# Performance work log

Measured on AMD Instinct MI355X. Metric: run time of the kernel, lower is better.

## Reference

```python
import jax, jax.numpy as jnp
import numpy as np

N, M = 1024, 32
FN, FE = 64, 32
AGG_N, AGG_E = 128, 64
OUT_N, OUT_E = 64, 32


def _build_indices(n, m):
    nip, eip = [], []
    k = 0
    for i in range(1, n):
        j0 = max(0, i - m)
        nip += list(range(j0, i))
        eip += list(range(k, k + i - j0))
        k += i - j0
    n1 = np.array(nip, np.int32)
    eT = np.array(eip, np.int32)
    n2 = np.concatenate([np.full(min(i, m), i, np.int32) for i in range(1, n)])
    # padded previous-node window indices (0 = zero pad slot)
    prev_nodes = np.zeros(n * m, np.int32)
    k = 0
    for i in range(n):
        t = min(i, m)
        prev_nodes[(i + 1) * m - t:(i + 1) * m] = np.arange(k, k + t) + 1
        k += t
    n_e = k
    norm_node = np.full(n, 1.0 / m, np.float32)
    for i in range(1, m):
        norm_node[i] = 1.0 / i
    prev_edges = np.zeros(n_e * m, np.int32)
    k = 0
    e = 0
    for i in range(n):
        j0 = max(0, i - m)
        for j in range(j0, i):
            if j > j0:
                prev_edges[(e + 1) * m - (j - j0):(e + 1) * m] = np.arange(k, k + j - j0) + 1
            e += 1
        k += i - j0
    norm_edge = np.ones(n_e, np.float32)
    k = 0
    for i in range(1, n):
        t = min(i, m)
        for j in range(t):
            if j > 0:
                norm_edge[k] = 1.0 / j
            k += 1
    return n1, eT, n2, prev_nodes, norm_node, prev_edges, norm_edge, n_e

N1, ET, N2, PREV_N, NORM_N, PREV_E, NORM_E, NE = _build_indices(N, M)
N1 = jnp.asarray(N1); ET = jnp.asarray(ET); N2 = jnp.asarray(N2)
PREV_N = jnp.asarray(PREV_N); PREV_E = jnp.asarray(PREV_E)
NORM_N = jnp.asarray(NORM_N); NORM_E = jnp.asarray(NORM_E)


def setup_inputs() -> dict:
    key = jax.random.key(0)
    ks = jax.random.split(key, 20)
    s = 0.02
    inp = {
        'input_nodes': jax.random.normal(ks[0], (2, N, FN), jnp.float32),
        'input_edges': jax.random.normal(ks[1], (2, NE, FE), jnp.float32),
        # node-branch MLPs (exclude_last=False)
        'Wan1': jax.random.normal(ks[2], (2 * FN + FE, 2 * AGG_N)) * s,
        'ban1': jnp.zeros((2 * AGG_N,)),
        'Wan2': jax.random.normal(ks[3], (2 * AGG_N, AGG_N)) * s,
        'ban2': jnp.zeros((AGG_N,)),
        'Wln1': jax.random.normal(ks[4], (AGG_N + FN, AGG_N + FN)) * s,
        'bln1': jnp.zeros((AGG_N + FN,)),
        'Wln2': jax.random.normal(ks[5], (AGG_N + FN, OUT_N)) * s,
        'bln2': jnp.zeros((OUT_N,)),
        # edge-branch MLPs
        'Wae1': jax.random.normal(ks[6], (FN + FE, 2 * AGG_E)) * s,
        'bae1': jnp.zeros((2 * AGG_E,)),
        'Wae2': jax.random.normal(ks[7], (2 * AGG_E, AGG_E)) * s,
        'bae2': jnp.zeros((AGG_E,)),
        'Wle1': jax.random.normal(ks[8], (AGG_E + FE, AGG_E + FE)) * s,
        'ble1': jnp.zeros((AGG_E + FE,)),
        'Wle2': jax.random.normal(ks[9], (AGG_E + FE, OUT_E)) * s,
        'ble2': jnp.zeros((OUT_E,)),
    }
    return inp


def _mlp2(x, W1, b1, W2, b2):
    return jax.nn.relu(jax.nn.relu(x @ W1 + b1) @ W2 + b2)


def reference(input_nodes, input_edges, Wan1, ban1, Wan2, ban2, Wln1, bln1, Wln2, bln2,
              Wae1, bae1, Wae2, bae2, Wle1, ble1, Wle2, ble2):
    B = input_nodes.shape[0]
    # gather node-edge pairs [B, NE, FN+FE] and node-edge-node triples [B, NE, 2FN+FE]
    pairs = jnp.concatenate([input_nodes[:, N1], input_edges[:, ET]], axis=-1)
    triples = jnp.concatenate([input_nodes[:, N1], input_edges[:, ET], input_nodes[:, N2]], axis=-1)
    # node branch (exclude_last=False -> triples)
    hn = _mlp2(triples, Wan1, ban1, Wan2, ban2)                     # [B, NE, AGG_N]
    hn = jnp.concatenate([jnp.zeros((B, 1, AGG_N), hn.dtype), hn], axis=1)
    pn = hn[:, PREV_N].reshape(B, N, M, AGG_N).sum(axis=2)          # padded window sum
    pn = pn * NORM_N[None, :, None]
    nodes_in = jnp.concatenate([pn, input_nodes], axis=-1)
    out_nodes = _mlp2(nodes_in, Wln1, bln1, Wln2, bln2)             # activation_nodes = relu
    # edge branch (pairs)
    he = _mlp2(pairs, Wae1, bae1, Wae2, bae2)                       # [B, NE, AGG_E]
    he = jnp.concatenate([jnp.zeros((B, 1, AGG_E), he.dtype), he], axis=1)
    pe = he[:, PREV_E].reshape(B, NE, M, AGG_E).sum(axis=2)
    pe = pe * NORM_E[None, :, None]
    edges_in = jnp.concatenate([pe, input_edges], axis=-1)
    out_edges = _mlp2(edges_in, Wle1, ble1, Wle2, ble2)             # activation_edges = relu
    return out_nodes, out_edges
```

## Files before the change

### kernel.cpp

```cpp
#include <hip/hip_runtime.h>
#include <cstdint>

#define NN    1024
#define MM    32
#define NEDGE 32240
#define MROWS 64480
#define PX    168
#define PST   392

typedef unsigned short ushort_t;

typedef __bf16 bf16x8 __attribute__((ext_vector_type(8)));
typedef float  floatx4 __attribute__((ext_vector_type(4)));

__device__ __forceinline__ float b2f(ushort_t u) {
    union { unsigned int i; float f; } v; v.i = ((unsigned int)u) << 16; return v.f;
}
__device__ __forceinline__ ushort_t f2b(float f) {
    unsigned int u = __builtin_bit_cast(unsigned int, f);
    u = (u + 0x7FFFu + ((u >> 16) & 1u)) >> 16;
    return (ushort_t)u;
}
__device__ __forceinline__ int edge_base(int i) {
    return (i <= MM) ? ((i * (i - 1)) >> 1) : (496 + (i - MM) * MM);
}
__device__ __forceinline__ void edge_ij(int e, int& i, int& j) {
    if (e < 496) {
        i = (int)((1.0f + sqrtf(8.0f * (float)e + 1.0f)) * 0.5f);
        while (((i * (i - 1)) >> 1) > e) --i;
        while (((i * (i + 1)) >> 1) <= e) ++i;
        j = e - ((i * (i - 1)) >> 1);
    } else {
        int q = e - 496;
        i = MM + (q >> 5);
        j = i - MM + (q & 31);
    }
}

__global__ __launch_bounds__(256) void k_pack(
        const float* an1, const float* an2, const float* ae1, const float* ae2,
        const float* le1, const float* le2, const float* ln1, const float* ln2,
        const float* nodes, const float* edges,
        ushort_t* pan1, ushort_t* pan2, ushort_t* pae1, ushort_t* pae2,
        ushort_t* ple1, ushort_t* ple2, ushort_t* pln1, ushort_t* pln2,
        ushort_t* nodesb, ushort_t* edgesb, int2* ijt) {
    __shared__ float tile[32][33];
    const int bid = blockIdx.x;
    const int tid = threadIdx.x;
    if (bid < 152) {
        const float* s; ushort_t* d; int K, N, t;
        if (bid < 40)       { s = an1; d = pan1; K = 160; N = 256; t = bid;       }
        else if (bid < 72)  { s = an2; d = pan2; K = 256; N = 128; t = bid - 40;  }
        else if (bid < 84)  { s = ae1; d = pae1; K = 96;  N = 128; t = bid - 72;  }
        else if (bid < 92)  { s = ae2; d = pae2; K = 128; N = 64;  t = bid - 84;  }
        else if (bid < 101) { s = le1; d = ple1; K = 96;  N = 96;  t = bid - 92;  }
        else if (bid < 104) { s = le2; d = ple2; K = 96;  N = 32;  t = bid - 101; }
        else if (bid < 140) { s = ln1; d = pln1; K = 192; N = 192; t = bid - 104; }
        else                { s = ln2; d = pln2; K = 192; N = 64;  t = bid - 140; }
        int ntn = N >> 5;
        int tk = t / ntn, tn = t - tk * ntn;
        int k0 = tk * 32, n0 = tn * 32;
        int tx = tid & 31, ty = tid >> 5;
#pragma unroll
        for (int m = 0; m < 4; ++m)
            tile[ty + m * 8][tx] = s[(size_t)(k0 + ty + m * 8) * N + n0 + tx];
        __syncthreads();
#pragma unroll
        for (int m = 0; m < 4; ++m)
            d[(size_t)(n0 + ty + m * 8) * K + k0 + tx] = f2b(tile[tx][ty + m * 8]);
    } else if (bid < 280) {
        int i4 = (bid - 152) * 256 + tid;
        float4 v = ((const float4*)nodes)[i4];
        uint2 o;
        o.x = (unsigned)f2b(v.x) | ((unsigned)f2b(v.y) << 16);
        o.y = (unsigned)f2b(v.z) | ((unsigned)f2b(v.w) << 16);
        ((uint2*)nodesb)[i4] = o;
    } else if (bid < 2296) {
        int i4 = (bid - 280) * 256 + tid;
        if (i4 < 515840) {
            float4 v = ((const float4*)edges)[i4];
            uint2 o;
            o.x = (unsigned)f2b(v.x) | ((unsigned)f2b(v.y) << 16);
            o.y = (unsigned)f2b(v.z) | ((unsigned)f2b(v.w) << 16);
            ((uint2*)edgesb)[i4] = o;
        }
    } else {
        int e = (bid - 2296) * 256 + tid;
        if (e < NEDGE) { int i, j; edge_ij(e, i, j); ijt[e] = make_int2(i, j); }
    }
}

__global__ __launch_bounds__(512, 2) void k_agg(
        const ushort_t* __restrict__ nodesb, const ushort_t* __restrict__ edgesb,
        const int2* __restrict__ ijt,
        const ushort_t* __restrict__ pan1, const float* __restrict__ ban1,
        const ushort_t* __restrict__ pan2, const float* __restrict__ ban2,
        const ushort_t* __restrict__ pae1, const float* __restrict__ bae1,
        const ushort_t* __restrict__ pae2, const float* __restrict__ bae2,
        ushort_t* __restrict__ hn, ushort_t* __restrict__ he) {
    __shared__ alignas(16) ushort_t X[32 * PX];
    __shared__ alignas(16) ushort_t H[32 * PST];
    const int tid = threadIdx.x;
    const int w = tid >> 6, l = tid & 63, lrow = l & 15, lq = l >> 4;
    const int mt = blockIdx.x;
    floatx4 zero = {0.f, 0.f, 0.f, 0.f};

    bf16x8 B0[5], B1[5], B2[3];
#pragma unroll
    for (int kt = 0; kt < 5; ++kt) {
        B0[kt] = *(const bf16x8*)(pan1 + (size_t)(16 * w + lrow) * 160 + kt * 32 + lq * 8);
        B1[kt] = *(const bf16x8*)(pan1 + (size_t)(16 * (w + 8) + lrow) * 160 + kt * 32 + lq * 8);
    }
#pragma unroll
    for (int kt = 0; kt < 3; ++kt)
        B2[kt] = *(const bf16x8*)(pae1 + (size_t)(16 * w + lrow) * 96 + kt * 32 + lq * 8);
    float c0 = ban1[16 * w + lrow];
    float c1 = ban1[16 * (w + 8) + lrow];
    float c2 = bae1[16 * w + lrow];

#pragma unroll
    for (int k = 0; k < 4; ++k) {
        int rr = w * 4 + k;
        int r = mt * 32 + rr;
        int off = (r >= NEDGE) ? 1 : 0;
        int2 ij = ijt[r - off * NEDGE];
        int bN = off * NN;
        unsigned* xr = (unsigned*)(X + rr * PX);
        const unsigned* nj = (const unsigned*)(nodesb + (size_t)(bN + ij.y) * 64);
        const unsigned* ni = (const unsigned*)(nodesb + (size_t)(bN + ij.x) * 64);
        const unsigned* eb = (const unsigned*)(edgesb + (size_t)r * 32);
        if (l < 32) { xr[l] = nj[l]; xr[48 + l] = ni[l]; }
        else        xr[l] = eb[l - 32];
    }
    __syncthreads();

#pragma unroll
    for (int s = 0; s < 2; ++s) {
        bf16x8 A[5];
#pragma unroll
        for (int kt = 0; kt < 5; ++kt)
            A[kt] = *(const bf16x8*)&X[(s * 16 + lrow) * PX + kt * 32 + lq * 8];
        floatx4 a0 = zero, a1 = zero, a2 = zero;
#pragma unroll
        for (int kt = 0; kt < 5; ++kt) {
            a0 = __builtin_amdgcn_mfma_f32_16x16x32_bf16(A[kt], B0[kt], a0, 0, 0, 0);
            a1 = __builtin_amdgcn_mfma_f32_16x16x32_bf16(A[kt], B1[kt], a1, 0, 0, 0);
        }
#pragma unroll
        for (int kt = 0; kt < 3; ++kt)
            a2 = __builtin_amdgcn_mfma_f32_16x16x32_bf16(A[kt], B2[kt], a2, 0, 0, 0);
#pragma unroll
        for (int r_ = 0; r_ < 4; ++r_) {
            int row = (s * 16 + lq * 4 + r_) * PST;
            H[row + 16 * w + lrow]       = f2b(fmaxf(a0[r_] + c0, 0.f));
            H[row + 128 + 16 * w + lrow] = f2b(fmaxf(a1[r_] + c1, 0.f));
            H[row + 256 + 16 * w + lrow] = f2b(fmaxf(a2[r_] + c2, 0.f));
        }
    }
    __syncthreads();

    floatx4 o0[2], o1[2];
    if (w < 4) {
        bf16x8 D0[8], D1[8];
#pragma unroll
        for (int kt = 0; kt < 8; ++kt) {
            D0[kt] = *(const bf16x8*)(pan2 + (size_t)(16 * w + lrow) * 256 + kt * 32 + lq * 8);
            D1[kt] = *(const bf16x8*)(pan2 + (size_t)(16 * (w + 4) + lrow) * 256 + kt * 32 + lq * 8);
        }
        float d0 = ban2[16 * w + lrow];
        float d1 = ban2[16 * (w + 4) + lrow];
#pragma unroll
        for (int s = 0; s < 2; ++s) {
            floatx4 a0 = zero, a1 = zero;
#pragma unroll
            for (int kt = 0; kt < 8; ++kt) {
                bf16x8 a = *(const bf16x8*)&H[(s * 16 + lrow) * PST + kt * 32 + lq * 8];
                a0 = __builtin_amdgcn_mfma_f32_16x16x32_bf16(a, D0[kt], a0, 0, 0, 0);
                a1 = __builtin_amdgcn_mfma_f32_16x16x32_bf16(a, D1[kt], a1, 0, 0, 0);
            }
#pragma unroll
            for (int r_ = 0; r_ < 4; ++r_) { o0[s][r_] = a0[r_] + d0; o1[s][r_] = a1[r_] + d1; }
        }
    } else {
        int u = w - 4;
        bf16x8 E[4];
#pragma unroll
        for (int kt = 0; kt < 4; ++kt)
            E[kt] = *(const bf16x8*)(pae2 + (size_t)(16 * u + lrow) * 128 + kt * 32 + lq * 8);
        float d2 = bae2[16 * u + lrow];
#pragma unroll
        for (int s = 0; s < 2; ++s) {
            floatx4 a2 = zero;
#pragma unroll
            for (int kt = 0; kt < 4; ++kt) {
                bf16x8 a = *(const bf16x8*)&H[(s * 16 + lrow) * PST + 256 + kt * 32 + lq * 8];
                a2 = __builtin_amdgcn_mfma_f32_16x16x32_bf16(a, E[kt], a2, 0, 0, 0);
            }
#pragma unroll
            for (int r_ = 0; r_ < 4; ++r_) o0[s][r_] = a2[r_] + d2;
        }
    }
    __syncthreads();

    ushort_t* S = X;
    ushort_t* T = H;
    if (w < 4) {
#pragma unroll
        for (int s = 0; s < 2; ++s)
#pragma unroll
            for (int r_ = 0; r_ < 4; ++r_) {
                int row = (s * 16 + lq * 4 + r_) * 136;
                S[row + 16 * w + lrow]        = f2b(fmaxf(o0[s][r_], 0.f));
                S[row + 64 + 16 * w + lrow]   = f2b(fmaxf(o1[s][r_], 0.f));
            }
    } else {
        int u = w - 4;
#pragma unroll
        for (int s = 0; s < 2; ++s)
#pragma unroll
            for (int r_ = 0; r_ < 4; ++r_)
                T[(s * 16 + lq * 4 + r_) * 72 + 16 * u + lrow] = f2b(fmaxf(o0[s][r_], 0.f));
    }
    __syncthreads();

    {
        int row = tid >> 4, c = tid & 15;
        ((uint4*)(hn + (size_t)(mt * 32 + row) * 128))[c] = *(const uint4*)&S[row * 136 + c * 8];
        if (tid < 256) {
            int row2 = tid >> 3, c2 = tid & 7;
            ((uint4*)(he + (size_t)(mt * 32 + row2) * 64))[c2] = *(const uint4*)&T[row2 * 72 + c2 * 8];
        }
    }
}

__global__ __launch_bounds__(256) void k_mid(
        const ushort_t* __restrict__ hn, const ushort_t* __restrict__ he,
        ushort_t* __restrict__ pn, ushort_t* __restrict__ pre) {
    const int tid = threadIdx.x;
    if (blockIdx.x < 2048) {
        int ri = blockIdx.x;
        int b = ri >> 10, i = ri & 1023;
        int t = min(i, MM);
        int base = b * NEDGE + edge_base(i);
        int c = tid & 63, g = tid >> 6;
        float s0 = 0.f, s1 = 0.f;
        for (int p = g; p < t; p += 4) {
            unsigned u = ((const unsigned*)(hn + (size_t)(base + p) * 128))[c];
            s0 += b2f((ushort_t)(u & 0xffff));
            s1 += b2f((ushort_t)(u >> 16));
        }
        __shared__ float red[4][128];
        red[g][c * 2] = s0; red[g][c * 2 + 1] = s1;
        __syncthreads();
        if (tid < 64) {
            float inv = 1.0f / (float)max(t, 1);
            float a0 = (red[0][tid * 2] + red[1][tid * 2] + red[2][tid * 2] + red[3][tid * 2]) * inv;
            float a1 = (red[0][tid * 2 + 1] + red[1][tid * 2 + 1] + red[2][tid * 2 + 1] + red[3][tid * 2 + 1]) * inv;
            ((unsigned*)(pn + (size_t)ri * 128))[tid] = (unsigned)f2b(a0) | ((unsigned)f2b(a1) << 16);
        }
    } else {
        int bi = blockIdx.x - 2048;
        int b = bi >> 10, i = bi & 1023;
        int t = min(i, MM);
        if (t == 0) return;
        int base = b * NEDGE + edge_base(i);
        __shared__ alignas(16) ushort_t hw[32 * 64];
        for (int u = tid; u < t * 8; u += 256)
            ((uint4*)hw)[u] = ((const uint4*)he)[(size_t)base * 8 + u];
        __syncthreads();
        if (tid < 64) {
            float run = 0.f;
            for (int p = 0; p < t; ++p) {
                float v = (p == 0) ? 0.f : run / (float)p;
                pre[(size_t)(base + p) * 64 + tid] = f2b(v);
                run += b2f(hw[p * 64 + tid]);
            }
        }
    }
}

__global__ __launch_bounds__(192) void k_final(
        const ushort_t* __restrict__ pn, const ushort_t* __restrict__ nodesb,
        const ushort_t* __restrict__ pln1, const float* __restrict__ bln1,
        const ushort_t* __restrict__ pln2, const float* __restrict__ bln2,
        float* __restrict__ out_nodes,
        const ushort_t* __restrict__ pre, const ushort_t* __restrict__ edgesb,
        const ushort_t* __restrict__ ple1, const float* __restrict__ ble1,
        const ushort_t* __restrict__ ple2, const float* __restrict__ ble2,
        float* __restrict__ out_edges) {
    __shared__ alignas(16) ushort_t LA[32 * 200];
    __shared__ alignas(16) ushort_t LB[32 * 200];
    const int tid = threadIdx.x;
    const int w = tid >> 6, l = tid & 63, lrow = l & 15, lq = l >> 4;
    floatx4 zero = {0.f, 0.f, 0.f, 0.f};

    if (blockIdx.x < 64) {
        int tile = blockIdx.x;
        for (int u = tid; u < 768; u += 192) {
            int row = u / 24, c = u - row * 24;
            int r = tile * 32 + row;
            const uint4* src = (c < 16) ? ((const uint4*)(pn + (size_t)r * 128) + c)
                                        : ((const uint4*)(nodesb + (size_t)r * 64) + (c - 16));
            *(uint4*)&LA[row * 200 + c * 8] = *src;
        }
        bf16x8 f1[6][4]; float v1[4];
#pragma unroll
        for (int kt = 0; kt < 6; ++kt)
#pragma unroll
            for (int nt = 0; nt < 4; ++nt)
                f1[kt][nt] = *(const bf16x8*)(pln1 + (size_t)(w * 64 + nt * 16 + lrow) * 192 + kt * 32 + lq * 8);
#pragma unroll
        for (int nt = 0; nt < 4; ++nt) v1[nt] = bln1[w * 64 + nt * 16 + lrow];
        __syncthreads();

        floatx4 acc[2][4];
#pragma unroll
        for (int s = 0; s < 2; ++s)
#pragma unroll
            for (int nt = 0; nt < 4; ++nt) acc[s][nt] = zero;
#pragma unroll
        for (int s = 0; s < 2; ++s)
#pragma unroll
            for (int kt = 0; kt < 6; ++kt) {
                bf16x8 a = *(const bf16x8*)&LA[(s * 16 + lrow) * 200 + kt * 32 + lq * 8];
#pragma unroll
                for (int nt = 0; nt < 4; ++nt)
                    acc[s][nt] = __builtin_amdgcn_mfma_f32_16x16x32_bf16(a, f1[kt][nt], acc[s][nt], 0, 0, 0);
            }
#pragma unroll
        for (int s = 0; s < 2; ++s)
#pragma unroll
            for (int nt = 0; nt < 4; ++nt) {
                int col = w * 64 + nt * 16 + lrow;
#pragma unroll
                for (int r_ = 0; r_ < 4; ++r_)
                    LB[(s * 16 + lq * 4 + r_) * 200 + col] = f2b(fmaxf(acc[s][nt][r_] + v1[nt], 0.f));
            }
        bf16x8 f2[6][2]; float v2[2] = {0.f, 0.f};
        if (w < 2) {
#pragma unroll
            for (int kt = 0; kt < 6; ++kt)
#pragma unroll
                for (int nt = 0; nt < 2; ++nt)
                    f2[kt][nt] = *(const bf16x8*)(pln2 + (size_t)(w * 32 + nt * 16 + lrow) * 192 + kt * 32 + lq * 8);
#pragma unroll
            for (int nt = 0; nt < 2; ++nt) v2[nt] = bln2[w * 32 + nt * 16 + lrow];
        }
        __syncthreads();
        if (w < 2) {
            floatx4 a2[2][2];
#pragma unroll
            for (int s = 0; s < 2; ++s) { a2[s][0] = zero; a2[s][1] = zero; }
#pragma unroll
            for (int s = 0; s < 2; ++s)
#pragma unroll
                for (int kt = 0; kt < 6; ++kt) {
                    bf16x8 a = *(const bf16x8*)&LB[(s * 16 + lrow) * 200 + kt * 32 + lq * 8];
#pragma unroll
                    for (int nt = 0; nt < 2; ++nt)
                        a2[s][nt] = __builtin_amdgcn_mfma_f32_16x16x32_bf16(a, f2[kt][nt], a2[s][nt], 0, 0, 0);
                }
#pragma unroll
            for (int s = 0; s < 2; ++s)
#pragma unroll
                for (int nt = 0; nt < 2; ++nt) {
                    int col = w * 32 + nt * 16 + lrow;
#pragma unroll
                    for (int r_ = 0; r_ < 4; ++r_)
                        out_nodes[(size_t)(tile * 32 + s * 16 + lq * 4 + r_) * 64 + col] =
                            fmaxf(a2[s][nt][r_] + v2[nt], 0.f);
                }
        }
    } else {
        int mt = blockIdx.x - 64;
        for (int u = tid; u < 384; u += 192) {
            int row = u / 12, c = u - row * 12;
            int r = mt * 32 + row;
            const uint4* src = (c < 8) ? ((const uint4*)(pre + (size_t)r * 64) + c)
                                       : ((const uint4*)(edgesb + (size_t)r * 32) + (c - 8));
            *(uint4*)&LA[row * 104 + c * 8] = *src;
        }
        bf16x8 fb1[3][2]; float v1[2];
#pragma unroll
        for (int kt = 0; kt < 3; ++kt)
#pragma unroll
            for (int nt = 0; nt < 2; ++nt)
                fb1[kt][nt] = *(const bf16x8*)(ple1 + (size_t)(w * 32 + nt * 16 + lrow) * 96 + kt * 32 + lq * 8);
#pragma unroll
        for (int nt = 0; nt < 2; ++nt) v1[nt] = ble1[w * 32 + nt * 16 + lrow];
        bf16x8 fb2[3]; float v2 = 0.f;
        if (w < 2) {
#pragma unroll
            for (int kt = 0; kt < 3; ++kt)
                fb2[kt] = *(const bf16x8*)(ple2 + (size_t)(w * 16 + lrow) * 96 + kt * 32 + lq * 8);
            v2 = ble2[w * 16 + lrow];
        }
        __syncthreads();

        floatx4 acc[2][2];
#pragma unroll
        for (int s = 0; s < 2; ++s) { acc[s][0] = zero; acc[s][1] = zero; }
#pragma unroll
        for (int s = 0; s < 2; ++s)
#pragma unroll
            for (int kt = 0; kt < 3; ++kt) {
                bf16x8 a = *(const bf16x8*)&LA[(s * 16 + lrow) * 104 + kt * 32 + lq * 8];
#pragma unroll
                for (int nt = 0; nt < 2; ++nt)
                    acc[s][nt] = __builtin_amdgcn_mfma_f32_16x16x32_bf16(a, fb1[kt][nt], acc[s][nt], 0, 0, 0);
            }
#pragma unroll
        for (int s = 0; s < 2; ++s)
#pragma unroll
            for (int nt = 0; nt < 2; ++nt) {
                int col = w * 32 + nt * 16 + lrow;
#pragma unroll
                for (int r_ = 0; r_ < 4; ++r_)
                    LB[(s * 16 + lq * 4 + r_) * 104 + col] = f2b(fmaxf(acc[s][nt][r_] + v1[nt], 0.f));
            }
        __syncthreads();
        if (w < 2) {
            floatx4 a2[2] = {zero, zero};
#pragma unroll
            for (int s = 0; s < 2; ++s)
#pragma unroll
                for (int kt = 0; kt < 3; ++kt) {
                    bf16x8 a = *(const bf16x8*)&LB[(s * 16 + lrow) * 104 + kt * 32 + lq * 8];
                    a2[s] = __builtin_amdgcn_mfma_f32_16x16x32_bf16(a, fb2[kt], a2[s], 0, 0, 0);
                }
#pragma unroll
            for (int s = 0; s < 2; ++s) {
                int col = w * 16 + lrow;
#pragma unroll
                for (int r_ = 0; r_ < 4; ++r_)
                    out_edges[(size_t)(mt * 32 + s * 16 + lq * 4 + r_) * 32 + col] = fmaxf(a2[s][r_] + v2, 0.f);
            }
        }
    }
}

extern "C" void kernel_launch(void* const* d_in, const int* in_sizes, int n_in,
                              void* d_out, int out_size, void* d_ws, size_t ws_size,
                              hipStream_t stream) {
    const float* nodes = (const float*)d_in[0];
    const float* edges = (const float*)d_in[1];
    const float* Wan1 = (const float*)d_in[2];  const float* ban1 = (const float*)d_in[3];
    const float* Wan2 = (const float*)d_in[4];  const float* ban2 = (const float*)d_in[5];
    const float* Wln1 = (const float*)d_in[6];  const float* bln1 = (const float*)d_in[7];
    const float* Wln2 = (const float*)d_in[8];  const float* bln2 = (const float*)d_in[9];
    const float* Wae1 = (const float*)d_in[10]; const float* bae1 = (const float*)d_in[11];
    const float* Wae2 = (const float*)d_in[12]; const float* bae2 = (const float*)d_in[13];
    const float* Wle1 = (const float*)d_in[14]; const float* ble1 = (const float*)d_in[15];
    const float* Wle2 = (const float*)d_in[16]; const float* ble2 = (const float*)d_in[17];

    char* ws = (char*)d_ws;
    size_t o = 0;
    auto alloc = [&](size_t bytes) -> void* {
        void* r = ws + o;
        o += (bytes + 255) & ~(size_t)255;
        return r;
    };
    ushort_t* hn     = (ushort_t*)alloc((size_t)MROWS * 128 * 2);
    ushort_t* he     = (ushort_t*)alloc((size_t)MROWS * 64 * 2);
    ushort_t* pre    = (ushort_t*)alloc((size_t)MROWS * 64 * 2);
    ushort_t* pn     = (ushort_t*)alloc((size_t)2048 * 128 * 2);
    ushort_t* nodesb = (ushort_t*)alloc((size_t)2 * NN * 64 * 2);
    ushort_t* edgesb = (ushort_t*)alloc((size_t)MROWS * 32 * 2);
    int2*     ijt    = (int2*)alloc((size_t)NEDGE * 8);
    ushort_t* pan1 = (ushort_t*)alloc(160 * 256 * 2);
    ushort_t* pan2 = (ushort_t*)alloc(256 * 128 * 2);
    ushort_t* pae1 = (ushort_t*)alloc(96 * 128 * 2);
    ushort_t* pae2 = (ushort_t*)alloc(128 * 64 * 2);
    ushort_t* ple1 = (ushort_t*)alloc(96 * 96 * 2);
    ushort_t* ple2 = (ushort_t*)alloc(96 * 32 * 2);
    ushort_t* pln1 = (ushort_t*)alloc(192 * 192 * 2);
    ushort_t* pln2 = (ushort_t*)alloc(192 * 64 * 2);

    float* out_nodes = (float*)d_out;
    float* out_edges = (float*)d_out + 2 * NN * 64;

    k_pack<<<2422, 256, 0, stream>>>(Wan1, Wan2, Wae1, Wae2, Wle1, Wle2, Wln1, Wln2,
                                     nodes, edges,
                                     pan1, pan2, pae1, pae2, ple1, ple2, pln1, pln2,
                                     nodesb, edgesb, ijt);
    k_agg<<<2015, 512, 0, stream>>>(nodesb, edgesb, ijt,
                                    pan1, ban1, pan2, ban2,
                                    pae1, bae1, pae2, bae2, hn, he);
    k_mid<<<4096, 256, 0, stream>>>(hn, he, pn, pre);
    k_final<<<64 + 2015, 192, 0, stream>>>(pn, nodesb, pln1, bln1, pln2, bln2, out_nodes,
                                           pre, edgesb, ple1, ble1, ple2, ble2, out_edges);

    (void)in_sizes; (void)n_in; (void)out_size; (void)ws_size;
}
```

Measured before the change: 168.1 us.

## Fuse entire edge branch into one per-node-window kernel, dropping he/pre buffers

Splits the edge MLP out of k_agg into a new k_edge kernel that handles one node window (up to 32 edges) per block. That kernel computes the first edge MLP, the prefix-mean aggregation and the final edge MLP entirely in shared memory, then writes out_edges directly. This removes the global round trips through the he and pre intermediates and shrinks k_agg, k_mid and k_final to the node branch only. In exchange, k_edge wastes MFMA work on partial windows (t<32), runs a serial per-lane prefix loop, and the node and edge branches now run as separate launches in sequence.

```diff
diff --git a/kernel.cpp b/kernel.cpp
--- a/kernel.cpp
+++ b/kernel.cpp
@@ -6,7 +6,7 @@
 #define NEDGE 32240
 #define MROWS 64480
 #define PX    168
-#define PST   392
+#define PSTN  264
 
 typedef unsigned short ushort_t;
 
@@ -95,28 +95,22 @@
         const int2* __restrict__ ijt,
         const ushort_t* __restrict__ pan1, const float* __restrict__ ban1,
         const ushort_t* __restrict__ pan2, const float* __restrict__ ban2,
-        const ushort_t* __restrict__ pae1, const float* __restrict__ bae1,
-        const ushort_t* __restrict__ pae2, const float* __restrict__ bae2,
-        ushort_t* __restrict__ hn, ushort_t* __restrict__ he) {
+        ushort_t* __restrict__ hn) {
     __shared__ alignas(16) ushort_t X[32 * PX];
-    __shared__ alignas(16) ushort_t H[32 * PST];
+    __shared__ alignas(16) ushort_t H[32 * PSTN];
     const int tid = threadIdx.x;
     const int w = tid >> 6, l = tid & 63, lrow = l & 15, lq = l >> 4;
     const int mt = blockIdx.x;
     floatx4 zero = {0.f, 0.f, 0.f, 0.f};
 
-    bf16x8 B0[5], B1[5], B2[3];
+    bf16x8 B0[5], B1[5];
 #pragma unroll
     for (int kt = 0; kt < 5; ++kt) {
         B0[kt] = *(const bf16x8*)(pan1 + (size_t)(16 * w + lrow) * 160 + kt * 32 + lq * 8);
         B1[kt] = *(const bf16x8*)(pan1 + (size_t)(16 * (w + 8) + lrow) * 160 + kt * 32 + lq * 8);
     }
-#pragma unroll
-    for (int kt = 0; kt < 3; ++kt)
-        B2[kt] = *(const bf16x8*)(pae1 + (size_t)(16 * w + lrow) * 96 + kt * 32 + lq * 8);
     float c0 = ban1[16 * w + lrow];
     float c1 = ban1[16 * (w + 8) + lrow];
-    float c2 = bae1[16 * w + lrow];
 
 #pragma unroll
     for (int k = 0; k < 4; ++k) {
@@ -140,142 +134,218 @@
 #pragma unroll
         for (int kt = 0; kt < 5; ++kt)
             A[kt] = *(const bf16x8*)&X[(s * 16 + lrow) * PX + kt * 32 + lq * 8];
-        floatx4 a0 = zero, a1 = zero, a2 = zero;
+        floatx4 a0 = zero, a1 = zero;
 #pragma unroll
         for (int kt = 0; kt < 5; ++kt) {
             a0 = __builtin_amdgcn_mfma_f32_16x16x32_bf16(A[kt], B0[kt], a0, 0, 0, 0);
             a1 = __builtin_amdgcn_mfma_f32_16x16x32_bf16(A[kt], B1[kt], a1, 0, 0, 0);
         }
 #pragma unroll
-        for (int kt = 0; kt < 3; ++kt)
-            a2 = __builtin_amdgcn_mfma_f32_16x16x32_bf16(A[kt], B2[kt], a2, 0, 0, 0);
-#pragma unroll
         for (int r_ = 0; r_ < 4; ++r_) {
-            int row = (s * 16 + lq * 4 + r_) * PST;
+            int row = (s * 16 + lq * 4 + r_) * PSTN;
             H[row + 16 * w + lrow]       = f2b(fmaxf(a0[r_] + c0, 0.f));
             H[row + 128 + 16 * w + lrow] = f2b(fmaxf(a1[r_] + c1, 0.f));
-            H[row + 256 + 16 * w + lrow] = f2b(fmaxf(a2[r_] + c2, 0.f));
-        }
-    }
-    __syncthreads();
-
-    floatx4 o0[2], o1[2];
-    if (w < 4) {
-        bf16x8 D0[8], D1[8];
-#pragma unroll
-        for (int kt = 0; kt < 8; ++kt) {
-            D0[kt] = *(const bf16x8*)(pan2 + (size_t)(16 * w + lrow) * 256 + kt * 32 + lq * 8);
-            D1[kt] = *(const bf16x8*)(pan2 + (size_t)(16 * (w + 4) + lrow) * 256 + kt * 32 + lq * 8);
-        }
+        }
+    }
+    __syncthreads();
+
+    {
+        bf16x8 D[8];
+#pragma unroll
+        for (int kt = 0; kt < 8; ++kt)
+            D[kt] = *(const bf16x8*)(pan2 + (size_t)(16 * w + lrow) * 256 + kt * 32 + lq * 8);
         float d0 = ban2[16 * w + lrow];
-        float d1 = ban2[16 * (w + 4) + lrow];
 #pragma unroll
         for (int s = 0; s < 2; ++s) {
-            floatx4 a0 = zero, a1 = zero;
+            floatx4 a0 = zero;
 #pragma unroll
             for (int kt = 0; kt < 8; ++kt) {
-                bf16x8 a = *(const bf16x8*)&H[(s * 16 + lrow) * PST + kt * 32 + lq * 8];
-                a0 = __builtin_amdgcn_mfma_f32_16x16x32_bf16(a, D0[kt], a0, 0, 0, 0);
-                a1 = __builtin_amdgcn_mfma_f32_16x16x32_bf16(a, D1[kt], a1, 0, 0, 0);
-            }
-#pragma unroll
-            for (int r_ = 0; r_ < 4; ++r_) { o0[s][r_] = a0[r_] + d0; o1[s][r_] = a1[r_] + d1; }
-        }
-    } else {
-        int u = w - 4;
+                bf16x8 a = *(const bf16x8*)&H[(s * 16 + lrow) * PSTN + kt * 32 + lq * 8];
+                a0 = __builtin_amdgcn_mfma_f32_16x16x32_bf16(a, D[kt], a0, 0, 0, 0);
+            }
+#pragma unroll
+            for (int r_ = 0; r_ < 4; ++r_)
+                X[(s * 16 + lq * 4 + r_) * 136 + 16 * w + lrow] = f2b(fmaxf(a0[r_] + d0, 0.f));
+        }
+    }
+    __syncthreads();
+
+    {
+        int row = tid >> 4, c = tid & 15;
+        ((uint4*)(hn + (size_t)(mt * 32 + row) * 128))[c] = *(const uint4*)&X[row * 136 + c * 8];
+    }
+}
+
+#define PXE 104
+#define PH1 136
+#define PHE 72
+__global__ __launch_bounds__(256) void k_edge(
+        const ushort_t* __restrict__ nodesb, const ushort_t* __restrict__ edgesb,
+        const ushort_t* __restrict__ pae1, const float* __restrict__ bae1,
+        const ushort_t* __restrict__ pae2, const float* __restrict__ bae2,
+        const ushort_t* __restrict__ ple1, const float* __restrict__ ble1,
+        const ushort_t* __restrict__ ple2, const float* __restrict__ ble2,
+        float* __restrict__ out_edges) {
+    __shared__ alignas(16) ushort_t X[32 * PXE];
+    __shared__ alignas(16) ushort_t H1[32 * PH1];
+    __shared__ alignas(16) ushort_t HE[32 * PHE];
+    __shared__ alignas(16) ushort_t LB[32 * PXE];
+    const int tid = threadIdx.x;
+    const int w = tid >> 6, l = tid & 63, lrow = l & 15, lq = l >> 4;
+    const int b = blockIdx.x >> 10, i = blockIdx.x & 1023;
+    const int t = min(i, MM);
+    if (t == 0) return;
+    const int j0 = i - t;
+    const int base = b * NEDGE + edge_base(i);
+    floatx4 zero = {0.f, 0.f, 0.f, 0.f};
+
+    bf16x8 B0[3], B1[3];
+#pragma unroll
+    for (int kt = 0; kt < 3; ++kt) {
+        B0[kt] = *(const bf16x8*)(pae1 + (size_t)(16 * w + lrow) * 96 + kt * 32 + lq * 8);
+        B1[kt] = *(const bf16x8*)(pae1 + (size_t)(16 * (w + 4) + lrow) * 96 + kt * 32 + lq * 8);
+    }
+    const float c0 = bae1[16 * w + lrow];
+    const float c1 = bae1[16 * (w + 4) + lrow];
+
+    for (int u = tid; u < 32 * 48; u += 256) {
+        int row = u / 48, c = u - row * 48;
+        unsigned v;
+        if (c < 32) v = ((const unsigned*)nodesb)[(size_t)(b * NN + j0 + row) * 32 + c];
+        else        v = ((const unsigned*)edgesb)[(size_t)(base + row) * 16 + (c - 32)];
+        ((unsigned*)X)[row * (PXE / 2) + c] = v;
+    }
+    __syncthreads();
+
+#pragma unroll
+    for (int s = 0; s < 2; ++s) {
+        bf16x8 A[3];
+#pragma unroll
+        for (int kt = 0; kt < 3; ++kt)
+            A[kt] = *(const bf16x8*)&X[(s * 16 + lrow) * PXE + kt * 32 + lq * 8];
+        floatx4 a0 = zero, a1 = zero;
+#pragma unroll
+        for (int kt = 0; kt < 3; ++kt) {
+            a0 = __builtin_amdgcn_mfma_f32_16x16x32_bf16(A[kt], B0[kt], a0, 0, 0, 0);
+            a1 = __builtin_amdgcn_mfma_f32_16x16x32_bf16(A[kt], B1[kt], a1, 0, 0, 0);
+        }
+#pragma unroll
+        for (int r_ = 0; r_ < 4; ++r_) {
+            int row = (s * 16 + lq * 4 + r_) * PH1;
+            H1[row + 16 * w + lrow]      = f2b(fmaxf(a0[r_] + c0, 0.f));
+            H1[row + 64 + 16 * w + lrow] = f2b(fmaxf(a1[r_] + c1, 0.f));
+        }
+    }
+    __syncthreads();
+
+    {
         bf16x8 E[4];
 #pragma unroll
         for (int kt = 0; kt < 4; ++kt)
-            E[kt] = *(const bf16x8*)(pae2 + (size_t)(16 * u + lrow) * 128 + kt * 32 + lq * 8);
-        float d2 = bae2[16 * u + lrow];
+            E[kt] = *(const bf16x8*)(pae2 + (size_t)(16 * w + lrow) * 128 + kt * 32 + lq * 8);
+        float d2 = bae2[16 * w + lrow];
 #pragma unroll
         for (int s = 0; s < 2; ++s) {
             floatx4 a2 = zero;
 #pragma unroll
             for (int kt = 0; kt < 4; ++kt) {
-                bf16x8 a = *(const bf16x8*)&H[(s * 16 + lrow) * PST + 256 + kt * 32 + lq * 8];
+                bf16x8 a = *(const bf16x8*)&H1[(s * 16 + lrow) * PH1 + kt * 32 + lq * 8];
                 a2 = __builtin_amdgcn_mfma_f32_16x16x32_bf16(a, E[kt], a2, 0, 0, 0);
             }
 #pragma unroll
-            for (int r_ = 0; r_ < 4; ++r_) o0[s][r_] = a2[r_] + d2;
-        }
-    }
-    __syncthreads();
-
-    ushort_t* S = X;
-    ushort_t* T = H;
-    if (w < 4) {
-#pragma unroll
-        for (int s = 0; s < 2; ++s)
+            for (int r_ = 0; r_ < 4; ++r_)
+                HE[(s * 16 + lq * 4 + r_) * PHE + 16 * w + lrow] = f2b(fmaxf(a2[r_] + d2, 0.f));
+        }
+    }
+    if (l < 16) {
+        float run = 0.f;
+        for (int p = 0; p < t; ++p) {
+            X[p * PXE + 16 * w + l] = f2b((p == 0) ? 0.f : run / (float)p);
+            run += b2f(HE[p * PHE + 16 * w + l]);
+        }
+    }
+    __syncthreads();
+
+    {
+        bf16x8 F0[3], F1[3];
+        const bool two = (w < 2);
+#pragma unroll
+        for (int kt = 0; kt < 3; ++kt) {
+            F0[kt] = *(const bf16x8*)(ple1 + (size_t)(16 * w + lrow) * 96 + kt * 32 + lq * 8);
+            if (two)
+                F1[kt] = *(const bf16x8*)(ple1 + (size_t)(16 * (w + 4) + lrow) * 96 + kt * 32 + lq * 8);
+        }
+        float v0 = ble1[16 * w + lrow];
+        float v1 = two ? ble1[16 * (w + 4) + lrow] : 0.f;
+#pragma unroll
+        for (int s = 0; s < 2; ++s) {
+            bf16x8 A[3];
+#pragma unroll
+            for (int kt = 0; kt < 3; ++kt)
+                A[kt] = *(const bf16x8*)&X[(s * 16 + lrow) * PXE + kt * 32 + lq * 8];
+            floatx4 a0 = zero, a1 = zero;
+#pragma unroll
+            for (int kt = 0; kt < 3; ++kt) {
+                a0 = __builtin_amdgcn_mfma_f32_16x16x32_bf16(A[kt], F0[kt], a0, 0, 0, 0);
+                if (two)
+                    a1 = __builtin_amdgcn_mfma_f32_16x16x32_bf16(A[kt], F1[kt], a1, 0, 0, 0);
+            }
 #pragma unroll
             for (int r_ = 0; r_ < 4; ++r_) {
-                int row = (s * 16 + lq * 4 + r_) * 136;
-                S[row + 16 * w + lrow]        = f2b(fmaxf(o0[s][r_], 0.f));
-                S[row + 64 + 16 * w + lrow]   = f2b(fmaxf(o1[s][r_], 0.f));
-            }
-    } else {
-        int u = w - 4;
-#pragma unroll
-        for (int s = 0; s < 2; ++s)
-#pragma unroll
-            for (int r_ = 0; r_ < 4; ++r_)
-                T[(s * 16 + lq * 4 + r_) * 72 + 16 * u + lrow] = f2b(fmaxf(o0[s][r_], 0.f));
+                int row = (s * 16 + lq * 4 + r_) * PXE;
+                LB[row + 16 * w + lrow] = f2b(fmaxf(a0[r_] + v0, 0.f));
+                if (two)
+                    LB[row + 64 + 16 * w + lrow] = f2b(fmaxf(a1[r_] + v1, 0.f));
+            }
+        }
     }
     __syncthreads();
 
     {
-        int row = tid >> 4, c = tid & 15;
-        ((uint4*)(hn + (size_t)(mt * 32 + row) * 128))[c] = *(const uint4*)&S[row * 136 + c * 8];
-        if (tid < 256) {
-            int row2 = tid >> 3, c2 = tid & 7;
-            ((uint4*)(he + (size_t)(mt * 32 + row2) * 64))[c2] = *(const uint4*)&T[row2 * 72 + c2 * 8];
+        int ct = w & 1, s = w >> 1;
+        int c0o = 16 * ct;
+        bf16x8 F2[3];
+#pragma unroll
+        for (int kt = 0; kt < 3; ++kt)
+            F2[kt] = *(const bf16x8*)(ple2 + (size_t)(c0o + lrow) * 96 + kt * 32 + lq * 8);
+        float v2 = ble2[c0o + lrow];
+        floatx4 a2 = zero;
+#pragma unroll
+        for (int kt = 0; kt < 3; ++kt) {
+            bf16x8 a = *(const bf16x8*)&LB[(s * 16 + lrow) * PXE + kt * 32 + lq * 8];
+            a2 = __builtin_amdgcn_mfma_f32_16x16x32_bf16(a, F2[kt], a2, 0, 0, 0);
+        }
+#pragma unroll
+        for (int r_ = 0; r_ < 4; ++r_) {
+            int grow = s * 16 + lq * 4 + r_;
+            if (grow < t)
+                out_edges[(size_t)(base + grow) * 32 + c0o + lrow] = fmaxf(a2[r_] + v2, 0.f);
         }
     }
 }
 
 __global__ __launch_bounds__(256) void k_mid(
-        const ushort_t* __restrict__ hn, const ushort_t* __restrict__ he,
-        ushort_t* __restrict__ pn, ushort_t* __restrict__ pre) {
+        const ushort_t* __restrict__ hn, ushort_t* __restrict__ pn) {
     const int tid = threadIdx.x;
-    if (blockIdx.x < 2048) {
-        int ri = blockIdx.x;
-        int b = ri >> 10, i = ri & 1023;
-        int t = min(i, MM);
-        int base = b * NEDGE + edge_base(i);
-        int c = tid & 63, g = tid >> 6;
-        float s0 = 0.f, s1 = 0.f;
-        for (int p = g; p < t; p += 4) {
-            unsigned u = ((const unsigned*)(hn + (size_t)(base + p) * 128))[c];
-            s0 += b2f((ushort_t)(u & 0xffff));
-            s1 += b2f((ushort_t)(u >> 16));
-        }
-        __shared__ float red[4][128];
-        red[g][c * 2] = s0; red[g][c * 2 + 1] = s1;
-        __syncthreads();
-        if (tid < 64) {
-            float inv = 1.0f / (float)max(t, 1);
-            float a0 = (red[0][tid * 2] + red[1][tid * 2] + red[2][tid * 2] + red[3][tid * 2]) * inv;
-            float a1 = (red[0][tid * 2 + 1] + red[1][tid * 2 + 1] + red[2][tid * 2 + 1] + red[3][tid * 2 + 1]) * inv;
-            ((unsigned*)(pn + (size_t)ri * 128))[tid] = (unsigned)f2b(a0) | ((unsigned)f2b(a1) << 16);
-        }
-    } else {
-        int bi = blockIdx.x - 2048;
-        int b = bi >> 10, i = bi & 1023;
-        int t = min(i, MM);
-        if (t == 0) return;
-        int base = b * NEDGE + edge_base(i);
-        __shared__ alignas(16) ushort_t hw[32 * 64];
-        for (int u = tid; u < t * 8; u += 256)
-            ((uint4*)hw)[u] = ((const uint4*)he)[(size_t)base * 8 + u];
-        __syncthreads();
-        if (tid < 64) {
-            float run = 0.f;
-            for (int p = 0; p < t; ++p) {
-                float v = (p == 0) ? 0.f : run / (float)p;
-                pre[(size_t)(base + p) * 64 + tid] = f2b(v);
-                run += b2f(hw[p * 64 + tid]);
-            }
-        }
+    int ri = blockIdx.x;
+    int b = ri >> 10, i = ri & 1023;
+    int t = min(i, MM);
+    int base = b * NEDGE + edge_base(i);
+    int c = tid & 63, g = tid >> 6;
+    float s0 = 0.f, s1 = 0.f;
+    for (int p = g; p < t; p += 4) {
+        unsigned u = ((const unsigned*)(hn + (size_t)(base + p) * 128))[c];
+        s0 += b2f((ushort_t)(u & 0xffff));
+        s1 += b2f((ushort_t)(u >> 16));
+    }
+    __shared__ float red[4][128];
+    red[g][c * 2] = s0; red[g][c * 2 + 1] = s1;
+    __syncthreads();
+    if (tid < 64) {
+        float inv = 1.0f / (float)max(t, 1);
+        float a0 = (red[0][tid * 2] + red[1][tid * 2] + red[2][tid * 2] + red[3][tid * 2]) * inv;
+        float a1 = (red[0][tid * 2 + 1] + red[1][tid * 2 + 1] + red[2][tid * 2 + 1] + red[3][tid * 2 + 1]) * inv;
+        ((unsigned*)(pn + (size_t)ri * 128))[tid] = (unsigned)f2b(a0) | ((unsigned)f2b(a1) << 16);
     }
 }
 
@@ -283,131 +353,77 @@
         const ushort_t* __restrict__ pn, const ushort_t* __restrict__ nodesb,
         const ushort_t* __restrict__ pln1, const float* __restrict__ bln1,
         const ushort_t* __restrict__ pln2, const float* __restrict__ bln2,
-        float* __restrict__ out_nodes,
-        const ushort_t* __restrict__ pre, const ushort_t* __restrict__ edgesb,
-        const ushort_t* __restrict__ ple1, const float* __restrict__ ble1,
-        const ushort_t* __restrict__ ple2, const float* __restrict__ ble2,
-        float* __restrict__ out_edges) {
+        float* __restrict__ out_nodes) {
     __shared__ alignas(16) ushort_t LA[32 * 200];
     __shared__ alignas(16) ushort_t LB[32 * 200];
     const int tid = threadIdx.x;
     const int w = tid >> 6, l = tid & 63, lrow = l & 15, lq = l >> 4;
     floatx4 zero = {0.f, 0.f, 0.f, 0.f};
 
-    if (blockIdx.x < 64) {
-        int tile = blockIdx.x;
-        for (int u = tid; u < 768; u += 192) {
-            int row = u / 24, c = u - row * 24;
-            int r = tile * 32 + row;
-            const uint4* src = (c < 16) ? ((const uint4*)(pn + (size_t)r * 128) + c)
-                                        : ((const uint4*)(nodesb + (size_t)r * 64) + (c - 16));
-            *(uint4*)&LA[row * 200 + c * 8] = *src;
-        }
-        bf16x8 f1[6][4]; float v1[4];
+    int tile = blockIdx.x;
+    for (int u = tid; u < 768; u += 192) {
+        int row = u / 24, c = u - row * 24;
+        int r = tile * 32 + row;
+        const uint4* src = (c < 16) ? ((const uint4*)(pn + (size_t)r * 128) + c)
+                                    : ((const uint4*)(nodesb + (size_t)r * 64) + (c - 16));
+        *(uint4*)&LA[row * 200 + c * 8] = *src;
+    }
+    bf16x8 f1[6][4]; float v1[4];
+#pragma unroll
+    for (int kt = 0; kt < 6; ++kt)
+#pragma unroll
+        for (int nt = 0; nt < 4; ++nt)
+            f1[kt][nt] = *(const bf16x8*)(pln1 + (size_t)(w * 64 + nt * 16 + lrow) * 192 + kt * 32 + lq * 8);
+#pragma unroll
+    for (int nt = 0; nt < 4; ++nt) v1[nt] = bln1[w * 64 + nt * 16 + lrow];
+    __syncthreads();
+
+    floatx4 acc[2][4];
+#pragma unroll
+    for (int s = 0; s < 2; ++s)
+#pragma unroll
+        for (int nt = 0; nt < 4; ++nt) acc[s][nt] = zero;
+#pragma unroll
+    for (int s = 0; s < 2; ++s)
+#pragma unroll
+        for (int kt = 0; kt < 6; ++kt) {
+            bf16x8 a = *(const bf16x8*)&LA[(s * 16 + lrow) * 200 + kt * 32 + lq * 8];
+#pragma unroll
+            for (int nt = 0; nt < 4; ++nt)
+                acc[s][nt] = __builtin_amdgcn_mfma_f32_16x16x32_bf16(a, f1[kt][nt], acc[s][nt], 0, 0, 0);
+        }
+#pragma unroll
+    for (int s = 0; s < 2; ++s)
+#pragma unroll
+        for (int nt = 0; nt < 4; ++nt) {
+            int col = w * 64 + nt * 16 + lrow;
+#pragma unroll
+            for (int r_ = 0; r_ < 4; ++r_)
+                LB[(s * 16 + lq * 4 + r_) * 200 + col] = f2b(fmaxf(acc[s][nt][r_] + v1[nt], 0.f));
+        }
+    bf16x8 f2[6][2]; float v2[2] = {0.f, 0.f};
+    if (w < 2) {
 #pragma unroll
         for (int kt = 0; kt < 6; ++kt)
 #pragma unroll
-            for (int nt = 0; nt < 4; ++nt)
-                f1[kt][nt] = *(const bf16x8*)(pln1 + (size_t)(w * 64 + nt * 16 + lrow) * 192 + kt * 32 + lq * 8);
-#pragma unroll
-        for (int nt = 0; nt < 4; ++nt) v1[nt] = bln1[w * 64 + nt * 16 + lrow];
-        __syncthreads();
-
-        floatx4 acc[2][4];
+            for (int nt = 0; nt < 2; ++nt)
+                f2[kt][nt] = *(const bf16x8*)(pln2 + (size_t)(w * 32 + nt * 16 + lrow) * 192 + kt * 32 + lq * 8);
+#pragma unroll
+        for (int nt = 0; nt < 2; ++nt) v2[nt] = bln2[w * 32 + nt * 16 + lrow];
+    }
+    __syncthreads();
+    if (w < 2) {
+        floatx4 a2[2][2];
+#pragma unroll
+        for (int s = 0; s < 2; ++s) { a2[s][0] = zero; a2[s][1] = zero; }
 #pragma unroll
         for (int s = 0; s < 2; ++s)
 #pragma unroll
-            for (int nt = 0; nt < 4; ++nt) acc[s][nt] = zero;
-#pragma unroll
-        for (int s = 0; s < 2; ++s)
-#pragma unroll
             for (int kt = 0; kt < 6; ++kt) {
-                bf16x8 a = *(const bf16x8*)&LA[(s * 16 + lrow) * 200 + kt * 32 + lq * 8];
-#pragma unroll
-                for (int nt = 0; nt < 4; ++nt)
-                    acc[s][nt] = __builtin_amdgcn_mfma_f32_16x16x32_bf16(a, f1[kt][nt], acc[s][nt], 0, 0, 0);
-            }
-#pragma unroll
-        for (int s = 0; s < 2; ++s)
-#pragma unroll
-            for (int nt = 0; nt < 4; ++nt) {
-                int col = w * 64 + nt * 16 + lrow;
-#pragma unroll
-                for (int r_ = 0; r_ < 4; ++r_)
-                    LB[(s * 16 + lq * 4 + r_) * 200 + col] = f2b(fmaxf(acc[s][nt][r_] + v1[nt], 0.f));
-            }
-        bf16x8 f2[6][2]; float v2[2] = {0.f, 0.f};
-        if (w < 2) {
-#pragma unroll
-            for (int kt = 0; kt < 6; ++kt)
+                bf16x8 a = *(const bf16x8*)&LB[(s * 16 + lrow) * 200 + kt * 32 + lq * 8];
 #pragma unroll
                 for (int nt = 0; nt < 2; ++nt)
-                    f2[kt][nt] = *(const bf16x8*)(pln2 + (size_t)(w * 32 + nt * 16 + lrow) * 192 + kt * 32 + lq * 8);
-#pragma unroll
-            for (int nt = 0; nt < 2; ++nt) v2[nt] = bln2[w * 32 + nt * 16 + lrow];
-        }
-        __syncthreads();
-        if (w < 2) {
-            floatx4 a2[2][2];
-#pragma unroll
-            for (int s = 0; s < 2; ++s) { a2[s][0] = zero; a2[s][1] = zero; }
-#pragma unroll
-            for (int s = 0; s < 2; ++s)
-#pragma unroll
-                for (int kt = 0; kt < 6; ++kt) {
-                    bf16x8 a = *(const bf16x8*)&LB[(s * 16 + lrow) * 200 + kt * 32 + lq * 8];
-#pragma unroll
-                    for (int nt = 0; nt < 2; ++nt)
-                        a2[s][nt] = __builtin_amdgcn_mfma_f32_16x16x32_bf16(a, f2[kt][nt], a2[s][nt], 0, 0, 0);
-                }
-#pragma unroll
-            for (int s = 0; s < 2; ++s)
-#pragma unroll
-                for (int nt = 0; nt < 2; ++nt) {
-                    int col = w * 32 + nt * 16 + lrow;
-#pragma unroll
-                    for (int r_ = 0; r_ < 4; ++r_)
-                        out_nodes[(size_t)(tile * 32 + s * 16 + lq * 4 + r_) * 64 + col] =
-                            fmaxf(a2[s][nt][r_] + v2[nt], 0.f);
-                }
-        }
-    } else {
-        int mt = blockIdx.x - 64;
-        for (int u = tid; u < 384; u += 192) {
-            int row = u / 12, c = u - row * 12;
-            int r = mt * 32 + row;
-            const uint4* src = (c < 8) ? ((const uint4*)(pre + (size_t)r * 64) + c)
-                                       : ((const uint4*)(edgesb + (size_t)r * 32) + (c - 8));
-            *(uint4*)&LA[row * 104 + c * 8] = *src;
-        }
-        bf16x8 fb1[3][2]; float v1[2];
-#pragma unroll
-        for (int kt = 0; kt < 3; ++kt)
-#pragma unroll
-            for (int nt = 0; nt < 2; ++nt)
-                fb1[kt][nt] = *(const bf16x8*)(ple1 + (size_t)(w * 32 + nt * 16 + lrow) * 96 + kt * 32 + lq * 8);
-#pragma unroll
-        for (int nt = 0; nt < 2; ++nt) v1[nt] = ble1[w * 32 + nt * 16 + lrow];
-        bf16x8 fb2[3]; float v2 = 0.f;
-        if (w < 2) {
-#pragma unroll
-            for (int kt = 0; kt < 3; ++kt)
-                fb2[kt] = *(const bf16x8*)(ple2 + (size_t)(w * 16 + lrow) * 96 + kt * 32 + lq * 8);
-            v2 = ble2[w * 16 + lrow];
-        }
-        __syncthreads();
-
-        floatx4 acc[2][2];
-#pragma unroll
-        for (int s = 0; s < 2; ++s) { acc[s][0] = zero; acc[s][1] = zero; }
-#pragma unroll
-        for (int s = 0; s < 2; ++s)
-#pragma unroll
-            for (int kt = 0; kt < 3; ++kt) {
-                bf16x8 a = *(const bf16x8*)&LA[(s * 16 + lrow) * 104 + kt * 32 + lq * 8];
-#pragma unroll
-                for (int nt = 0; nt < 2; ++nt)
-                    acc[s][nt] = __builtin_amdgcn_mfma_f32_16x16x32_bf16(a, fb1[kt][nt], acc[s][nt], 0, 0, 0);
+                    a2[s][nt] = __builtin_amdgcn_mfma_f32_16x16x32_bf16(a, f2[kt][nt], a2[s][nt], 0, 0, 0);
             }
 #pragma unroll
         for (int s = 0; s < 2; ++s)
@@ -416,26 +432,9 @@
                 int col = w * 32 + nt * 16 + lrow;
 #pragma unroll
                 for (int r_ = 0; r_ < 4; ++r_)
-                    LB[(s * 16 + lq * 4 + r_) * 104 + col] = f2b(fmaxf(acc[s][nt][r_] + v1[nt], 0.f));
-            }
-        __syncthreads();
-        if (w < 2) {
-            floatx4 a2[2] = {zero, zero};
-#pragma unroll
-            for (int s = 0; s < 2; ++s)
-#pragma unroll
-                for (int kt = 0; kt < 3; ++kt) {
-                    bf16x8 a = *(const bf16x8*)&LB[(s * 16 + lrow) * 104 + kt * 32 + lq * 8];
-                    a2[s] = __builtin_amdgcn_mfma_f32_16x16x32_bf16(a, fb2[kt], a2[s], 0, 0, 0);
-                }
-#pragma unroll
-            for (int s = 0; s < 2; ++s) {
-                int col = w * 16 + lrow;
-#pragma unroll
-                for (int r_ = 0; r_ < 4; ++r_)
-                    out_edges[(size_t)(mt * 32 + s * 16 + lq * 4 + r_) * 32 + col] = fmaxf(a2[s][r_] + v2, 0.f);
-            }
-        }
+                    out_nodes[(size_t)(tile * 32 + s * 16 + lq * 4 + r_) * 64 + col] =
+                        fmaxf(a2[s][nt][r_] + v2[nt], 0.f);
+            }
     }
 }
 
@@ -461,8 +460,6 @@
         return r;
     };
     ushort_t* hn     = (ushort_t*)alloc((size_t)MROWS * 128 * 2);
-    ushort_t* he     = (ushort_t*)alloc((size_t)MROWS * 64 * 2);
-    ushort_t* pre    = (ushort_t*)alloc((size_t)MROWS * 64 * 2);
     ushort_t* pn     = (ushort_t*)alloc((size_t)2048 * 128 * 2);
     ushort_t* nodesb = (ushort_t*)alloc((size_t)2 * NN * 64 * 2);
     ushort_t* edgesb = (ushort_t*)alloc((size_t)MROWS * 32 * 2);
@@ -484,11 +481,12 @@
                                      pan1, pan2, pae1, pae2, ple1, ple2, pln1, pln2,
                                      nodesb, edgesb, ijt);
     k_agg<<<2015, 512, 0, stream>>>(nodesb, edgesb, ijt,
-                                    pan1, ban1, pan2, ban2,
-                                    pae1, bae1, pae2, bae2, hn, he);
-    k_mid<<<4096, 256, 0, stream>>>(hn, he, pn, pre);
-    k_final<<<64 + 2015, 192, 0, stream>>>(pn, nodesb, pln1, bln1, pln2, bln2, out_nodes,
-                                           pre, edgesb, ple1, ble1, ple2, ble2, out_edges);
+                                    pan1, ban1, pan2, ban2, hn);
+    k_edge<<<2048, 256, 0, stream>>>(nodesb, edgesb,
+                                     pae1, bae1, pae2, bae2,
+                                     ple1, ble1, ple2, ble2, out_edges);
+    k_mid<<<2048, 256, 0, stream>>>(hn, pn);
+    k_final<<<64, 192, 0, stream>>>(pn, nodesb, pln1, bln1, pln2, bln2, out_nodes);
 
     (void)in_sizes; (void)n_in; (void)out_size; (void)ws_size;
 }
```

Measured after the change: 171.5 us. 1.02x slower.
